# Kernel optimization log

Measured on AMD Instinct MI355X. Metric: run time of the kernel, lower is better.

Reference implementation:

```python
import jax, jax.numpy as jnp
import numpy as np

N, CH, H, W = 2, 64, 96, 96
NH, CHUNK, RED = 4, 144, 4
CM = CH // RED  # match channels = 16
RES_SCALE = 1.0
NORM_EPS = 5e-5


def conv2d(x, w, b):
    # 3x3 'same' conv, NCHW / OIHW
    y = jax.lax.conv_general_dilated(x, w, (1, 1), 'SAME',
                                     dimension_numbers=('NCHW', 'OIHW', 'NCHW'))
    return y + b[None, :, None, None]


def setup_inputs() -> dict:
    key = jax.random.key(0)
    ks = jax.random.split(key, 8)
    L = H * W
    hb = min(L // CHUNK + (L // CHUNK) % 2, 128)  # = 64
    x = jax.random.normal(ks[0], (N, CH, H, W), jnp.float32)
    # per-round semi-orthogonal rotations: rows of (CM, hb) orthonormal
    g = jax.random.normal(ks[1], (NH, hb, CM), jnp.float32)
    q = jnp.stack([jnp.linalg.qr(g[h])[0] for h in range(NH)])  # (NH, hb, CM)
    rot = jnp.transpose(q, (2, 0, 1))  # (CM, NH, hb)
    def s(k, shape, fan):
        return jax.random.normal(k, shape, jnp.float32) / np.sqrt(fan).astype(np.float32)
    wm = s(ks[2], (CM, CH, 3, 3), CH * 9)
    wa = s(ks[3], (CH, CH, 3, 3), CH * 9)
    wf = s(ks[4], (CH, CH, 3, 3), CH * 9)
    fc1_w = s(ks[5], (CHUNK, CH), CH)
    fc2_w = s(ks[6], (CHUNK, CHUNK), CHUNK)
    return {'x': x, 'rot': rot,
            'wm': wm, 'bm': jnp.zeros((CM,), jnp.float32),
            'wa': wa, 'ba': jnp.zeros((CH,), jnp.float32),
            'wf': wf, 'bf': jnp.zeros((CH,), jnp.float32),
            'fc1_w': fc1_w, 'fc1_b': jnp.zeros((CHUNK,), jnp.float32),
            'fc2_w': fc2_w, 'fc2_b': jnp.zeros((CHUNK,), jnp.float32)}


def reference(x, rot, wm, bm, wa, ba, wf, bf, fc1_w, fc1_b, fc2_w, fc2_b):
    n, _, h, w = x.shape
    L = h * w
    hb = rot.shape[-1]
    # embeddings: (N, L, C)
    xe = jax.nn.relu(conv2d(x, wm, bm)).reshape(n, CM, L).transpose(0, 2, 1)
    ye = jax.nn.relu(conv2d(x, wa, ba)).reshape(n, CH, L).transpose(0, 2, 1)
    fe = jax.nn.relu(conv2d(x, wf, bf)).reshape(n, CH, L).transpose(0, 2, 1)
    # LSH: argmax over rotated directions, offset per round (detached in original)
    rv = jnp.einsum('ntf,fhi->nhti', xe, rot)  # (N, NH, L, hb)
    codes = jnp.argmax(rv, -1) + (jnp.arange(NH) * hb)[None, :, None]
    codes = codes.reshape(n, NH * L)
    idx = jnp.argsort(codes, axis=-1)
    undo = jnp.argsort(idx, axis=-1)
    mod = idx % L
    gather = lambda t: jnp.take_along_axis(t, mod[..., None], axis=1)
    nch = L // CHUNK  # L chosen divisible by CHUNK -> padding = 0
    xs = gather(xe).reshape(n, NH, nch, CHUNK, CM)
    ys = gather(ye).reshape(n, NH, nch, CHUNK, CH)
    fs = gather(fe).reshape(n, NH, nch, CHUNK, CH)
    nrm = jnp.linalg.norm(xs, axis=-1, keepdims=True)
    xmatch = xs / jnp.maximum(nrm, NORM_EPS)
    adj = lambda t: jnp.concatenate([t, jnp.roll(t, 1, axis=2), jnp.roll(t, -1, axis=2)], axis=3)
    xmatch = adj(xmatch)   # (n, NH, nch, 3*CHUNK, CM)
    ya = adj(ys)           # (n, NH, nch, 3*CHUNK, CH)
    fa = adj(fs)           # (n, NH, nch, 3*CHUNK, CH)
    hid = jax.nn.relu(fa @ fc1_w.T + fc1_b)
    fc_raw = jnp.swapaxes(hid @ fc2_w.T + fc2_b, -1, -2)  # (n, NH, nch, CHUNK, 3*CHUNK)
    raw = jnp.einsum('nhkie,nhkje->nhkij', xs, xmatch) + fc_raw
    bsc = jax.scipy.special.logsumexp(raw, axis=-1, keepdims=True)
    score = jnp.exp(raw - bsc)
    ret = jnp.einsum('nhkij,nhkje->nhkie', score, ya)  # (n, NH, nch, CHUNK, CH)
    ret = ret.reshape(n, NH * L, CH)
    bsc = bsc.reshape(n, NH * L)
    ret = jnp.take_along_axis(ret, undo[..., None], axis=1)
    bsc = jnp.take_along_axis(bsc, undo, axis=1)
    ret = ret.reshape(n, NH, L, CH)
    probs = jax.nn.softmax(bsc.reshape(n, NH, L, 1), axis=1)
    out = jnp.sum(ret * probs, axis=1)  # (n, L, CH)
    out = out.transpose(0, 2, 1).reshape(n, CH, h, w)
    return out * RES_SCALE + x
```

## Files before the change

### kernel.cpp

```cpp
#include <hip/hip_runtime.h>
#include <hip/hip_bf16.h>

#define LL 9216
#define TOT 36864
#define CHK 144
#define NSEG 144
#define EPS_N 5e-5f

typedef __bf16 bf16x8 __attribute__((ext_vector_type(8)));
typedef float f32x4 __attribute__((ext_vector_type(4)));

__device__ __forceinline__ float dot4(float4 a, float4 b) {
    return a.x*b.x + a.y*b.y + a.z*b.z + a.w*b.w;
}
__device__ __forceinline__ unsigned short f2bf(float f) {
    __hip_bfloat16 h = __float2bfloat16(f);
    return *reinterpret_cast<unsigned short*>(&h);
}
__device__ __forceinline__ float bf2f(unsigned short u) {
    return __uint_as_float(((unsigned int)u) << 16);
}

__global__ __launch_bounds__(256) void k_wprep(
    const float* __restrict__ fc1w, const float* __restrict__ fc2w,
    const float* __restrict__ wa, const float* __restrict__ wf,
    unsigned short* __restrict__ w1bf, unsigned short* __restrict__ w2bf,
    unsigned short* __restrict__ wpack)
{
    int i = blockIdx.x * 256 + threadIdx.x;
    if (i < 144 * 64) w1bf[i] = f2bf(fc1w[i]);
    if (i < 144 * 160) {
        int r = i / 160, c = i - r * 160;
        w2bf[i] = (c < 144) ? f2bf(fc2w[r * 144 + c]) : 0;
    }
    if (i < 128 * 576) {
        int o = i / 576, kk = i - o * 576;
        int dydx = kk >> 6, c = kk & 63;
        const float* src = (o < 64) ? wa : wf;
        wpack[i] = f2bf(src[(o & 63) * 576 + c * 9 + dydx]);
    }
}

__global__ __launch_bounds__(256) void k_conv2(
    const float* __restrict__ x, const float* __restrict__ wm,
    const float* __restrict__ bm, const float* __restrict__ rot,
    unsigned short* __restrict__ xeb, unsigned short* __restrict__ xnb,
    unsigned char* __restrict__ codes,
    const unsigned short* __restrict__ wpack,
    const float* __restrict__ ba, const float* __restrict__ bfb,
    const unsigned short* __restrict__ w1bf, const float* __restrict__ fc1_b,
    const unsigned short* __restrict__ w2bf, const float* __restrict__ fc2_b,
    unsigned short* __restrict__ yeb, unsigned short* __restrict__ re2b)
{
    __shared__ __align__(16) char smem[47104];
    int tid = threadIdx.x;
    int b7 = blockIdx.x % 7, bq = blockIdx.x / 7;

    if (b7 < 3) {
        float* xl   = (float*)smem;
        float* rotT = (float*)(smem + 25600);
        float* xsp  = (float*)(smem + 41984);
        int b = bq * 3 + b7;
        int n = b / 144, tile = b % 144;
        int ty0 = (tile / 12) * 8, tx0 = (tile % 12) * 8;
        for (int li = tid; li < 6400; li += 256) {
            int c = li / 100, s = li % 100;
            int yy = s / 10, xx = s % 10;
            int gy = ty0 + yy - 1, gx = tx0 + xx - 1;
            float v = 0.f;
            if ((unsigned)gy < 96u && (unsigned)gx < 96u)
                v = x[((n * 64 + c) * 96 + gy) * 96 + gx];
            xl[li] = v;
        }
        for (int e = tid; e < 4096; e += 256) {
            int f = e >> 8, r = e & 255;
            rotT[r * 16 + f] = rot[f * 256 + r];
        }
        __syncthreads();
        int p = tid & 63, og = tid >> 6;
        int row = p >> 3, col = p & 7;
        int ogs = __builtin_amdgcn_readfirstlane(og);
        const float* wb = wm + (size_t)ogs * 4 * 576;
        float acc0 = 0.f, acc1 = 0.f, acc2 = 0.f, acc3 = 0.f;
        for (int c = 0; c < 64; ++c) {
            float xp[9];
            int base = c * 100 + row * 10 + col;
            #pragma unroll
            for (int dy = 0; dy < 3; ++dy)
                #pragma unroll
                for (int dx = 0; dx < 3; ++dx)
                    xp[dy * 3 + dx] = xl[base + dy * 10 + dx];
            const float* w0 = wb + c * 9;
            #pragma unroll
            for (int u = 0; u < 9; ++u) {
                acc0 += w0[u]        * xp[u];
                acc1 += w0[576 + u]  * xp[u];
                acc2 += w0[1152 + u] * xp[u];
                acc3 += w0[1728 + u] * xp[u];
            }
        }
        int o = ogs * 4;
        float v0 = acc0 + bm[o + 0]; v0 = v0 > 0.f ? v0 : 0.f;
        float v1 = acc1 + bm[o + 1]; v1 = v1 > 0.f ? v1 : 0.f;
        float v2 = acc2 + bm[o + 2]; v2 = v2 > 0.f ? v2 : 0.f;
        float v3 = acc3 + bm[o + 3]; v3 = v3 > 0.f ? v3 : 0.f;
        size_t t = (size_t)n * LL + (ty0 + row) * 96 + tx0 + col;
        unsigned short pk[4] = {f2bf(v0), f2bf(v1), f2bf(v2), f2bf(v3)};
        *(uint2*)(xeb + t * 16 + o) = *(uint2*)pk;
        *(float4*)(xsp + p * 20 + o) = make_float4(v0, v1, v2, v3);
        __syncthreads();
        int pos = tid & 63, h = tid >> 6;
        int prow = pos >> 3, pcol = pos & 7;
        size_t tc = (size_t)n * LL + (ty0 + prow) * 96 + tx0 + pcol;
        float4 q0 = *(float4*)(xsp + pos * 20 + 0);
        float4 q1 = *(float4*)(xsp + pos * 20 + 4);
        float4 q2 = *(float4*)(xsp + pos * 20 + 8);
        float4 q3 = *(float4*)(xsp + pos * 20 + 12);
        if (h == 0) {
            float nn = dot4(q0,q0) + dot4(q1,q1) + dot4(q2,q2) + dot4(q3,q3);
            float s = fmaxf(sqrtf(nn), EPS_N);
            float inv = 1.f / s;
            unsigned short pn[16];
            pn[0]=f2bf(q0.x*inv);  pn[1]=f2bf(q0.y*inv);  pn[2]=f2bf(q0.z*inv);  pn[3]=f2bf(q0.w*inv);
            pn[4]=f2bf(q1.x*inv);  pn[5]=f2bf(q1.y*inv);  pn[6]=f2bf(q1.z*inv);  pn[7]=f2bf(q1.w*inv);
            pn[8]=f2bf(q2.x*inv);  pn[9]=f2bf(q2.y*inv);  pn[10]=f2bf(q2.z*inv); pn[11]=f2bf(q2.w*inv);
            pn[12]=f2bf(q3.x*inv); pn[13]=f2bf(q3.y*inv); pn[14]=f2bf(q3.z*inv); pn[15]=f2bf(q3.w*inv);
            *(uint4*)(xnb + tc * 16)     = ((uint4*)pn)[0];
            *(uint4*)(xnb + tc * 16 + 8) = ((uint4*)pn)[1];
        }
        float best = -1e30f; int bi = 0;
        const float* rp = rotT + h * 1024;
        for (int i = 0; i < 64; ++i) {
            const float4* r4 = (const float4*)(rp + i * 16);
            float v = dot4(q0, r4[0]) + dot4(q1, r4[1]) + dot4(q2, r4[2]) + dot4(q3, r4[3]);
            if (v > best) { best = v; bi = i; }
        }
        codes[(size_t)n * TOT + h * LL + (tc - (size_t)n * LL)] = (unsigned char)(h * 64 + bi);
        return;
    }

    unsigned short* xt  = (unsigned short*)smem;
    unsigned short* fet = (unsigned short*)(smem + 21600);
    unsigned short* hb  = (unsigned short*)(smem + 28512);
    int b = bq * 4 + (b7 - 3);
    int n = b / 192, rem = b % 192;
    int y = rem >> 1, strip = rem & 1;
    int x0 = strip * 48;
    for (int e = tid; e < 9600; e += 256) {
        int r = e / 3200, r2 = e - r * 3200;
        int c = r2 / 50, j = r2 - c * 50;
        int gy = y - 1 + r, gx = x0 - 1 + j;
        float v = 0.f;
        if ((unsigned)gy < 96u && (unsigned)gx < 96u)
            v = x[((n * 64 + c) * 96 + gy) * 96 + gx];
        xt[(r * 50 + j) * 72 + c] = f2bf(v);
    }
    for (int e = tid; e < 384; e += 256) {
        int r = e >> 3, pq = e & 7;
        *(unsigned int*)(hb + r * 168 + 144 + pq * 2) = 0;
    }
    __syncthreads();
    int wave = tid >> 6, lane = tid & 63;
    int n16 = lane & 15, quad = lane >> 4;
    f32x4 acc[2][3];
    #pragma unroll
    for (int mi = 0; mi < 2; ++mi)
        #pragma unroll
        for (int nt = 0; nt < 3; ++nt) acc[mi][nt] = (f32x4){0.f, 0.f, 0.f, 0.f};
    #pragma unroll
    for (int s = 0; s < 18; ++s) {
        int dydx = s >> 1, half = s & 1;
        int dy = dydx / 3, dxm = dydx - dy * 3;
        bf16x8 B[3];
        #pragma unroll
        for (int nt = 0; nt < 3; ++nt) {
            int j = nt * 16 + n16 + dxm;
            B[nt] = *(bf16x8*)(xt + (dy * 50 + j) * 72 + half * 32 + quad * 8);
        }
        #pragma unroll
        for (int mi = 0; mi < 2; ++mi) {
            int o = (wave * 2 + mi) * 16 + n16;
            bf16x8 A = *(const bf16x8*)(wpack + o * 576 + dydx * 64 + half * 32 + quad * 8);
            #pragma unroll
            for (int nt = 0; nt < 3; ++nt)
                acc[mi][nt] = __builtin_amdgcn_mfma_f32_16x16x32_bf16(A, B[nt], acc[mi][nt], 0, 0, 0);
        }
    }
    #pragma unroll
    for (int mi = 0; mi < 2; ++mi) {
        int mt = wave * 2 + mi;
        int obase = mt * 16 + quad * 4;
        float4 b4 = (mt < 4) ? *(const float4*)(ba + obase)
                             : *(const float4*)(bfb + obase - 64);
        #pragma unroll
        for (int nt = 0; nt < 3; ++nt) {
            int j = nt * 16 + n16;
            unsigned short pk[4];
            float v0 = acc[mi][nt][0] + b4.x; pk[0] = f2bf(v0 > 0.f ? v0 : 0.f);
            float v1 = acc[mi][nt][1] + b4.y; pk[1] = f2bf(v1 > 0.f ? v1 : 0.f);
            float v2 = acc[mi][nt][2] + b4.z; pk[2] = f2bf(v2 > 0.f ? v2 : 0.f);
            float v3 = acc[mi][nt][3] + b4.w; pk[3] = f2bf(v3 > 0.f ? v3 : 0.f);
            if (mt < 4) {
                size_t t = (size_t)n * LL + y * 96 + x0 + j;
                *(uint2*)(yeb + t * 64 + obase) = *(uint2*)pk;
            } else {
                *(uint2*)(fet + j * 72 + (obase - 64)) = *(uint2*)pk;
            }
        }
    }
    __syncthreads();
    size_t R0 = (size_t)n * LL + y * 96 + x0;
    for (int nt = wave; nt < 9; nt += 4) {
        int bn = nt * 16 + n16;
        bf16x8 b0 = *(const bf16x8*)(w1bf + bn * 64 + quad * 8);
        bf16x8 b1 = *(const bf16x8*)(w1bf + bn * 64 + 32 + quad * 8);
        float bb = fc1_b[bn];
        #pragma unroll
        for (int m = 0; m < 3; ++m) {
            int arow = m * 16 + n16;
            bf16x8 a0 = *(bf16x8*)(fet + arow * 72 + quad * 8);
            bf16x8 a1 = *(bf16x8*)(fet + arow * 72 + 32 + quad * 8);
            f32x4 c2 = {0.f, 0.f, 0.f, 0.f};
            c2 = __builtin_amdgcn_mfma_f32_16x16x32_bf16(a0, b0, c2, 0, 0, 0);
            c2 = __builtin_amdgcn_mfma_f32_16x16x32_bf16(a1, b1, c2, 0, 0, 0);
            #pragma unroll
            for (int r = 0; r < 4; ++r) {
                float v = c2[r] + bb;
                hb[(m * 16 + quad * 4 + r) * 168 + bn] = f2bf(v > 0.f ? v : 0.f);
            }
        }
    }
    __syncthreads();
    for (int nt = wave; nt < 9; nt += 4) {
        int bn = nt * 16 + n16;
        bf16x8 wv2[5];
        #pragma unroll
        for (int kk = 0; kk < 5; ++kk)
            wv2[kk] = *(const bf16x8*)(w2bf + bn * 160 + kk * 32 + quad * 8);
        float bb = fc2_b[bn];
        #pragma unroll
        for (int m = 0; m < 3; ++m) {
            int arow = m * 16 + n16;
            f32x4 c2 = {0.f, 0.f, 0.f, 0.f};
            #pragma unroll
            for (int kk = 0; kk < 5; ++kk) {
                bf16x8 a = *(bf16x8*)(hb + arow * 168 + kk * 32 + quad * 8);
                c2 = __builtin_amdgcn_mfma_f32_16x16x32_bf16(a, wv2[kk], c2, 0, 0, 0);
            }
            #pragma unroll
            for (int r = 0; r < 4; ++r)
                re2b[(R0 + m * 16 + quad * 4 + r) * 144 + bn] = f2bf(c2[r] + bb);
        }
    }
}

__global__ __launch_bounds__(256) void k_hist(
    const unsigned char* __restrict__ codes, int* __restrict__ hist)
{
    __shared__ int lh[256];
    int b2 = blockIdx.x;
    int n = b2 / NSEG, seg = b2 % NSEG;
    int tid = threadIdx.x;
    lh[tid] = 0;
    __syncthreads();
    int code = codes[(size_t)n * TOT + seg * 256 + tid];
    atomicAdd(&lh[code], 1);
    __syncthreads();
    hist[((size_t)n * 256 + tid) * NSEG + seg] = lh[tid];
}

__global__ void k_scan(int* __restrict__ hist)
{
    __shared__ int sc[256];
    int n = blockIdx.x, bin = threadIdx.x;
    int* hp = hist + ((size_t)n * 256 + bin) * NSEG;
    int4 buf[36];
    int4* hp4 = (int4*)hp;
    #pragma unroll
    for (int q = 0; q < 36; ++q) buf[q] = hp4[q];
    int running = 0;
    #pragma unroll
    for (int q = 0; q < 36; ++q) {
        int t0 = buf[q].x; buf[q].x = running; running += t0;
        int t1 = buf[q].y; buf[q].y = running; running += t1;
        int t2 = buf[q].z; buf[q].z = running; running += t2;
        int t3 = buf[q].w; buf[q].w = running; running += t3;
    }
    sc[bin] = running;
    __syncthreads();
    for (int off = 1; off < 256; off <<= 1) {
        int v = sc[bin];
        int u = (bin >= off) ? sc[bin - off] : 0;
        __syncthreads();
        sc[bin] = v + u;
        __syncthreads();
    }
    int bs = sc[bin] - running;
    #pragma unroll
    for (int q = 0; q < 36; ++q) {
        buf[q].x += bs; buf[q].y += bs; buf[q].z += bs; buf[q].w += bs;
        hp4[q] = buf[q];
    }
}

__global__ __launch_bounds__(256) void k_place(
    const unsigned char* __restrict__ codes, const int* __restrict__ hist,
    int* __restrict__ idx)
{
    __shared__ unsigned char cl[256];
    int b = blockIdx.x, n = b / NSEG, seg = b % NSEG;
    int tid = threadIdx.x;
    int my = codes[(size_t)n * TOT + seg * 256 + tid];
    cl[tid] = (unsigned char)my;
    __syncthreads();
    int rank = 0;
    for (int j = 0; j < tid; ++j) rank += (cl[j] == my);
    int pos = hist[((size_t)n * 256 + my) * NSEG + seg] + rank;
    idx[(size_t)n * TOT + pos] = seg * 256 + tid;
}

__global__ __launch_bounds__(256) void k_gather(
    const int* __restrict__ idx, const unsigned short* __restrict__ xeb,
    const unsigned short* __restrict__ xnb, const unsigned short* __restrict__ yeb,
    const unsigned short* __restrict__ re2b,
    unsigned short* __restrict__ qs, unsigned short* __restrict__ ks,
    unsigned short* __restrict__ vsT, unsigned short* __restrict__ fst,
    int* __restrict__ undo)
{
    __shared__ int tl[144];
    int b0 = blockIdx.x;
    int b = ((b0 & 7) << 6) | (b0 >> 3);
    int nh = b >> 6, chunk = b & 63;
    int n = nh >> 2, h = nh & 3;
    size_t gb = (size_t)nh * LL + chunk * 144;
    size_t nL = (size_t)n * LL;
    int tid = threadIdx.x;
    if (tid < 144) {
        int t = idx[(size_t)n * TOT + h * LL + chunk * 144 + tid] - h * LL;
        tl[tid] = t;
        undo[(size_t)nh * LL + t] = chunk * 144 + tid;
    }
    __syncthreads();
    for (int e = tid; e < 288; e += 256) {
        int s = e >> 1, half = e & 1;
        size_t src = (nL + tl[s]) * 16 + half * 8;
        *(uint4*)(qs + (gb + s) * 16 + half * 8) = *(const uint4*)(xeb + src);
        *(uint4*)(ks + (gb + s) * 16 + half * 8) = *(const uint4*)(xnb + src);
    }
    size_t vb = (size_t)(nh * 64 + chunk) * 64;
    for (int e = tid; e < 576; e += 256) {
        int p = e % 72, su = e / 72;
        uint4 a  = *(const uint4*)(yeb + (nL + tl[2 * p])     * 64 + su * 8);
        uint4 bq = *(const uint4*)(yeb + (nL + tl[2 * p + 1]) * 64 + su * 8);
        const unsigned short* pa = (const unsigned short*)&a;
        const unsigned short* pb = (const unsigned short*)&bq;
        #pragma unroll
        for (int ci = 0; ci < 8; ++ci) {
            int c = su * 8 + ci;
            *(unsigned int*)(vsT + (vb + c) * 144 + 2 * p) =
                (unsigned int)pa[ci] | ((unsigned int)pb[ci] << 16);
        }
    }
    for (int e = tid; e < 1296; e += 256) {
        int mt = e / 144, s = e - mt * 144;
        const unsigned short* src = re2b + (nL + tl[s]) * 144 + mt * 16;
        unsigned short* dst = fst + ((size_t)(nh * 9 + mt) * LL + chunk * 144 + s) * 16;
        *(uint4*)(dst)     = *(const uint4*)(src);
        *(uint4*)(dst + 8) = *(const uint4*)(src + 8);
    }
}

__global__ __launch_bounds__(256, 2) void k_attn(
    const unsigned short* __restrict__ qs, const unsigned short* __restrict__ ks,
    const unsigned short* __restrict__ vsT, const unsigned short* __restrict__ fst,
    unsigned short* __restrict__ rets, float* __restrict__ bscs)
{
    __shared__ __align__(16) unsigned short Pw[4][16 * 56];

    int B = blockIdx.x;
    int wb = (B & 7) * 144 + (B >> 3);
    int tid = threadIdx.x;
    int lane = tid & 63, wv = tid >> 6;
    int n16 = lane & 15, quad = lane >> 4;
    int job = wb * 4 + wv;
    int bucket = job / 9, mt = job - bucket * 9;
    int n = bucket >> 8, rem = bucket & 255;
    int h = rem >> 6, k = rem & 63;
    int nh = n * 4 + h;

    size_t hL = (size_t)nh * LL;
    int ch0 = k, ch1 = (k + 63) & 63, ch2 = (k + 1) & 63;
    unsigned short* Pp = &Pw[wv][0];
    const unsigned short* fsl = fst + (size_t)(nh * 9 + mt) * LL * 16;

    bf16x8 afragQ = {};
    if (quad < 2)
        afragQ = *(const bf16x8*)(qs + (hL + ch0 * 144 + mt * 16 + n16) * 16 + quad * 8);

    f32x4 acc[4];
    float rm[4], rl[4];
    #pragma unroll
    for (int ct = 0; ct < 4; ++ct) acc[ct] = (f32x4){0.f, 0.f, 0.f, 0.f};
    #pragma unroll
    for (int r = 0; r < 4; ++r) { rm[r] = -1e30f; rl[r] = 0.f; }

#define SLOT(T) ((((T) < 3) ? ch0 : ((T) < 6) ? ch1 : ch2) * 144 + ((T) % 3) * 48)

#define LOAD_KF(T, KS, FV) do {                                                      \
    int sl_ = SLOT(T);                                                               \
    if (quad < 2) {                                                                  \
        KS[0] = *(const bf16x8*)(ks + (hL + sl_ + n16) * 16 + quad * 8);             \
        KS[1] = *(const bf16x8*)(ks + (hL + sl_ + 16 + n16) * 16 + quad * 8);        \
        KS[2] = *(const bf16x8*)(ks + (hL + sl_ + 32 + n16) * 16 + quad * 8);        \
    }                                                                                \
    FV[0] = *(const ushort4*)(fsl + (size_t)(sl_ + n16) * 16 + quad * 4);            \
    FV[1] = *(const ushort4*)(fsl + (size_t)(sl_ + 16 + n16) * 16 + quad * 4);       \
    FV[2] = *(const ushort4*)(fsl + (size_t)(sl_ + 32 + n16) * 16 + quad * 4);       \
} while (0)

#define ATTN_ITER(T, KS, FV, NKS, NFV) do {                                          \
    int chx_ = ((T) < 3) ? ch0 : ((T) < 6) ? ch1 : ch2;                              \
    const unsigned short* vch_ = vsT + (size_t)(nh * 64 + chx_) * 9216;              \
    int vo_ = ((T) % 3) * 48;                                                        \
    bf16x8 Bv0_[4];                                                                  \
    _Pragma("unroll")                                                                \
    for (int ct_ = 0; ct_ < 4; ++ct_)                                                \
        Bv0_[ct_] = *(const bf16x8*)(vch_ + (size_t)(ct_ * 16 + n16) * 144 + vo_ + quad * 8); \
    if ((T) < 8) LOAD_KF((T) + 1, NKS, NFV);                                         \
    f32x4 c0_ = {bf2f(FV[0].x), bf2f(FV[0].y), bf2f(FV[0].z), bf2f(FV[0].w)};        \
    f32x4 c1_ = {bf2f(FV[1].x), bf2f(FV[1].y), bf2f(FV[1].z), bf2f(FV[1].w)};        \
    f32x4 c2_ = {bf2f(FV[2].x), bf2f(FV[2].y), bf2f(FV[2].z), bf2f(FV[2].w)};        \
    c0_ = __builtin_amdgcn_mfma_f32_16x16x32_bf16(afragQ, KS[0], c0_, 0, 0, 0);      \
    c1_ = __builtin_amdgcn_mfma_f32_16x16x32_bf16(afragQ, KS[1], c1_, 0, 0, 0);      \
    c2_ = __builtin_amdgcn_mfma_f32_16x16x32_bf16(afragQ, KS[2], c2_, 0, 0, 0);      \
    _Pragma("unroll")                                                                \
    for (int r_ = 0; r_ < 4; ++r_) {                                                 \
        float v0_ = c0_[r_], v1_ = c1_[r_], v2_ = c2_[r_];                           \
        float mm_ = fmaxf(fmaxf(v0_, v1_), v2_);                                     \
        mm_ = fmaxf(mm_, __shfl_xor(mm_, 1, 16));                                    \
        mm_ = fmaxf(mm_, __shfl_xor(mm_, 2, 16));                                    \
        mm_ = fmaxf(mm_, __shfl_xor(mm_, 4, 16));                                    \
        mm_ = fmaxf(mm_, __shfl_xor(mm_, 8, 16));                                    \
        float mn_ = fmaxf(rm[r_], mm_);                                              \
        float a_ = __expf(rm[r_] - mn_);                                             \
        float s0_ = __expf(v0_ - mn_), s1_ = __expf(v1_ - mn_), s2_ = __expf(v2_ - mn_); \
        float ss_ = s0_ + s1_ + s2_;                                                 \
        ss_ += __shfl_xor(ss_, 1, 16);                                               \
        ss_ += __shfl_xor(ss_, 2, 16);                                               \
        ss_ += __shfl_xor(ss_, 4, 16);                                               \
        ss_ += __shfl_xor(ss_, 8, 16);                                               \
        rl[r_] = rl[r_] * a_ + ss_;                                                  \
        rm[r_] = mn_;                                                                \
        acc[0][r_] *= a_; acc[1][r_] *= a_; acc[2][r_] *= a_; acc[3][r_] *= a_;      \
        int rw_ = quad * 4 + r_;                                                     \
        Pp[rw_ * 56 +      n16] = f2bf(s0_);                                         \
        Pp[rw_ * 56 + 16 + n16] = f2bf(s1_);                                         \
        Pp[rw_ * 56 + 32 + n16] = f2bf(s2_);                                         \
    }                                                                                \
                \
    bf16x8 Ap0_ = *(const bf16x8*)(Pp + n16 * 56 + quad * 8);                        \
    int ko1_ = (quad < 2) ? 32 + quad * 8 : 0;          \
    bf16x8 Bv1_[4];                                                                  \
    _Pragma("unroll")                                                                \
    for (int ct_ = 0; ct_ < 4; ++ct_)                                                \
        Bv1_[ct_] = *(const bf16x8*)(vch_ + (size_t)(ct_ * 16 + n16) * 144 + vo_ + ko1_); \
    _Pragma("unroll")                                                                \
    for (int ct_ = 0; ct_ < 4; ++ct_)                                                \
        acc[ct_] = __builtin_amdgcn_mfma_f32_16x16x32_bf16(Ap0_, Bv0_[ct_], acc[ct_], 0, 0, 0); \
    bf16x8 Ap1_ = {};                                                                \
    if (quad < 2)                                                                    \
        Ap1_ = *(const bf16x8*)(Pp + n16 * 56 + 32 + quad * 8);                      \
    _Pragma("unroll")                                                                \
    for (int ct_ = 0; ct_ < 4; ++ct_)                                                \
        acc[ct_] = __builtin_amdgcn_mfma_f32_16x16x32_bf16(Ap1_, Bv1_[ct_], acc[ct_], 0, 0, 0); \
} while (0)

    bf16x8 ksA[3] = {}, ksB[3] = {};
    ushort4 fvA[3], fvB[3];
    LOAD_KF(0, ksA, fvA);
    ATTN_ITER(0, ksA, fvA, ksB, fvB);
    ATTN_ITER(1, ksB, fvB, ksA, fvA);
    ATTN_ITER(2, ksA, fvA, ksB, fvB);
    ATTN_ITER(3, ksB, fvB, ksA, fvA);
    ATTN_ITER(4, ksA, fvA, ksB, fvB);
    ATTN_ITER(5, ksB, fvB, ksA, fvA);
    ATTN_ITER(6, ksA, fvA, ksB, fvB);
    ATTN_ITER(7, ksB, fvB, ksA, fvA);
    ATTN_ITER(8, ksA, fvA, ksB, fvB);

#undef ATTN_ITER
#undef LOAD_KF
#undef SLOT

    size_t sp0 = hL + ch0 * 144;
    if (n16 == 0) {
        #pragma unroll
        for (int r = 0; r < 4; ++r)
            bscs[sp0 + mt * 16 + quad * 4 + r] = rm[r] + __logf(rl[r]);
    }
    #pragma unroll
    for (int r = 0; r < 4; ++r) {
        float inv = 1.f / rl[r];
        #pragma unroll
        for (int ct = 0; ct < 4; ++ct)
            rets[(sp0 + mt * 16 + quad * 4 + r) * 64 + ct * 16 + n16] =
                f2bf(acc[ct][r] * inv);
    }
}

__global__ __launch_bounds__(256) void k_final(
    const unsigned short* __restrict__ rets, const float* __restrict__ bscs,
    const int* __restrict__ undo, const float* __restrict__ x,
    float* __restrict__ out)
{
    __shared__ float pr[4][64];
    __shared__ int us[4][64];
    __shared__ float accl[64 * 65];
    int b = blockIdx.x, n = b / 144;
    int t0 = (b % 144) * 64;
    int tid = threadIdx.x;
    {
        int h = tid >> 6, tt = tid & 63;
        us[h][tt] = undo[((size_t)n * 4 + h) * LL + t0 + tt];
    }
    __syncthreads();
    if (tid < 64) {
        float b0 = bscs[((size_t)n * 4 + 0) * LL + us[0][tid]];
        float b1 = bscs[((size_t)n * 4 + 1) * LL + us[1][tid]];
        float b2 = bscs[((size_t)n * 4 + 2) * LL + us[2][tid]];
        float b3 = bscs[((size_t)n * 4 + 3) * LL + us[3][tid]];
        float mx = fmaxf(fmaxf(b0, b1), fmaxf(b2, b3));
        float e0 = __expf(b0-mx), e1 = __expf(b1-mx), e2 = __expf(b2-mx), e3 = __expf(b3-mx);
        float inv = 1.f / (e0 + e1 + e2 + e3);
        pr[0][tid] = e0*inv; pr[1][tid] = e1*inv; pr[2][tid] = e2*inv; pr[3][tid] = e3*inv;
    }
    __syncthreads();
    int cc = tid & 63, tt4 = tid >> 6;
    #pragma unroll
    for (int q = 0; q < 16; ++q) {
        int tt = tt4 + 4*q;
        float v = 0.f;
        #pragma unroll
        for (int h2 = 0; h2 < 4; ++h2)
            v += bf2f(rets[(((size_t)n*4 + h2)*LL + us[h2][tt])*64 + cc]) * pr[h2][tt];
        accl[cc*65 + tt] = v;
    }
    __syncthreads();
    int tt = tid & 63, c4 = tid >> 6;
    #pragma unroll
    for (int q = 0; q < 16; ++q) {
        int ch = c4 + 4*q;
        size_t o = ((size_t)n*64 + ch)*LL + t0 + tt;
        out[o] = accl[ch*65 + tt] + x[o];
    }
}

extern "C" void kernel_launch(void* const* d_in, const int* in_sizes, int n_in,
                              void* d_out, int out_size, void* d_ws, size_t ws_size,
                              hipStream_t stream)
{
    const float* x    = (const float*)d_in[0];
    const float* rot  = (const float*)d_in[1];
    const float* wm   = (const float*)d_in[2];
    const float* bm   = (const float*)d_in[3];
    const float* wa   = (const float*)d_in[4];
    const float* ba   = (const float*)d_in[5];
    const float* wf   = (const float*)d_in[6];
    const float* bf   = (const float*)d_in[7];
    const float* fc1w = (const float*)d_in[8];
    const float* fc1b = (const float*)d_in[9];
    const float* fc2w = (const float*)d_in[10];
    const float* fc2b = (const float*)d_in[11];
    float* out = (float*)d_out;

    char* ws = (char*)d_ws;
    unsigned short* xeb  = (unsigned short*)(ws + 0);
    unsigned short* yeb  = (unsigned short*)(ws + 589824);
    unsigned short* xnb  = (unsigned short*)(ws + 2949120);
    unsigned short* re2b = (unsigned short*)(ws + 3538944);
    unsigned short* w1bf = (unsigned short*)(ws + 8847360);
    unsigned short* w2bf = (unsigned short*)(ws + 8865792);
    unsigned short* wpak = (unsigned short*)(ws + 8911872);
    unsigned char* codes = (unsigned char*)(ws + 9059328);
    int* hist            = (int*)(ws + 9133056);
    int* idxb            = (int*)(ws + 9427968);
    unsigned short* rets = (unsigned short*)(ws + 0);
    float* bscs          = (float*)(ws + 9437184);
    unsigned short* qs   = (unsigned short*)(ws + 9732096);
    unsigned short* ks   = (unsigned short*)(ws + 12091392);
    unsigned short* vsT  = (unsigned short*)(ws + 14450688);
    unsigned short* fst  = (unsigned short*)(ws + 23887872);
    int* undo            = (int*)(ws + 45121536);

    k_wprep    <<<288,  256, 0, stream>>>(fc1w, fc2w, wa, wf, w1bf, w2bf, wpak);
    k_conv2    <<<672,  256, 0, stream>>>(x, wm, bm, rot, xeb, xnb, codes,
                                          wpak, ba, bf, w1bf, fc1b, w2bf, fc2b,
                                          yeb, re2b);
    k_hist     <<<288,  256, 0, stream>>>(codes, hist);
    k_scan     <<<2,    256, 0, stream>>>(hist);
    k_place    <<<288,  256, 0, stream>>>(codes, hist, idxb);
    k_gather   <<<512,  256, 0, stream>>>(idxb, xeb, xnb, yeb, re2b,
                                          qs, ks, vsT, fst, undo);
    k_attn     <<<1152, 256, 0, stream>>>(qs, ks, vsT, fst, rets, bscs);
    k_final    <<<288,  256, 0, stream>>>(rets, bscs, undo, x, out);
}
```

Before: 201.9 us.

## Split gather and final kernels across more blocks; per-wave rank histograms in place

k_place now builds per-wavefront code histograms in shared memory, so each thread counts matches only within its own wave instead of scanning all earlier threads. k_gather is split into two block halves, one copying q/k/v and the other copying the fc tiles and undo indices, which doubles the grid. k_final handles 16 tokens per block instead of 64, quadrupling the grid to raise parallelism. The narrower k_final tiles make the output stores only 16 floats wide per channel row, which reduces coalescing, and the gather split re-reads the idx/tl setup in both halves.

```diff
diff --git a/kernel.cpp b/kernel.cpp
--- a/kernel.cpp
+++ b/kernel.cpp
@@ -269,7 +269,7 @@
     hist[((size_t)n * 256 + tid) * NSEG + seg] = lh[tid];
 }
 
-__global__ void k_scan(int* __restrict__ hist)
+__global__ __launch_bounds__(256, 1) void k_scan(int* __restrict__ hist)
 {
     __shared__ int sc[256];
     int n = blockIdx.x, bin = threadIdx.x;
@@ -308,13 +308,20 @@
     int* __restrict__ idx)
 {
     __shared__ unsigned char cl[256];
+    __shared__ int wh[4][256];
     int b = blockIdx.x, n = b / NSEG, seg = b % NSEG;
-    int tid = threadIdx.x;
+    int tid = threadIdx.x, wv = tid >> 6;
+    for (int e = tid; e < 1024; e += 256) ((int*)wh)[e] = 0;
     int my = codes[(size_t)n * TOT + seg * 256 + tid];
     cl[tid] = (unsigned char)my;
     __syncthreads();
+    atomicAdd(&wh[wv][my], 1);
+    __syncthreads();
     int rank = 0;
-    for (int j = 0; j < tid; ++j) rank += (cl[j] == my);
+    for (int j = wv << 6; j < tid; ++j) rank += (cl[j] == my);
+    #pragma unroll
+    for (int w = 0; w < 3; ++w)
+        if (w < wv) rank += wh[w][my];
     int pos = hist[((size_t)n * 256 + my) * NSEG + seg] + rank;
     idx[(size_t)n * TOT + pos] = seg * 256 + tid;
 }
@@ -329,7 +336,8 @@
 {
     __shared__ int tl[144];
     int b0 = blockIdx.x;
-    int b = ((b0 & 7) << 6) | (b0 >> 3);
+    int half = b0 >> 9, bb = b0 & 511;
+    int b = ((bb & 7) << 6) | (bb >> 3);
     int nh = b >> 6, chunk = b & 63;
     int n = nh >> 2, h = nh & 3;
     size_t gb = (size_t)nh * LL + chunk * 144;
@@ -338,35 +346,38 @@
     if (tid < 144) {
         int t = idx[(size_t)n * TOT + h * LL + chunk * 144 + tid] - h * LL;
         tl[tid] = t;
-        undo[(size_t)nh * LL + t] = chunk * 144 + tid;
-    }
-    __syncthreads();
-    for (int e = tid; e < 288; e += 256) {
-        int s = e >> 1, half = e & 1;
-        size_t src = (nL + tl[s]) * 16 + half * 8;
-        *(uint4*)(qs + (gb + s) * 16 + half * 8) = *(const uint4*)(xeb + src);
-        *(uint4*)(ks + (gb + s) * 16 + half * 8) = *(const uint4*)(xnb + src);
-    }
-    size_t vb = (size_t)(nh * 64 + chunk) * 64;
-    for (int e = tid; e < 576; e += 256) {
-        int p = e % 72, su = e / 72;
-        uint4 a  = *(const uint4*)(yeb + (nL + tl[2 * p])     * 64 + su * 8);
-        uint4 bq = *(const uint4*)(yeb + (nL + tl[2 * p + 1]) * 64 + su * 8);
-        const unsigned short* pa = (const unsigned short*)&a;
-        const unsigned short* pb = (const unsigned short*)&bq;
-        #pragma unroll
-        for (int ci = 0; ci < 8; ++ci) {
-            int c = su * 8 + ci;
-            *(unsigned int*)(vsT + (vb + c) * 144 + 2 * p) =
-                (unsigned int)pa[ci] | ((unsigned int)pb[ci] << 16);
-        }
-    }
-    for (int e = tid; e < 1296; e += 256) {
-        int mt = e / 144, s = e - mt * 144;
-        const unsigned short* src = re2b + (nL + tl[s]) * 144 + mt * 16;
-        unsigned short* dst = fst + ((size_t)(nh * 9 + mt) * LL + chunk * 144 + s) * 16;
-        *(uint4*)(dst)     = *(const uint4*)(src);
-        *(uint4*)(dst + 8) = *(const uint4*)(src + 8);
+        if (half) undo[(size_t)nh * LL + t] = chunk * 144 + tid;
+    }
+    __syncthreads();
+    if (!half) {
+        for (int e = tid; e < 288; e += 256) {
+            int s = e >> 1, hf = e & 1;
+            size_t src = (nL + tl[s]) * 16 + hf * 8;
+            *(uint4*)(qs + (gb + s) * 16 + hf * 8) = *(const uint4*)(xeb + src);
+            *(uint4*)(ks + (gb + s) * 16 + hf * 8) = *(const uint4*)(xnb + src);
+        }
+        size_t vb = (size_t)(nh * 64 + chunk) * 64;
+        for (int e = tid; e < 576; e += 256) {
+            int p = e % 72, su = e / 72;
+            uint4 a  = *(const uint4*)(yeb + (nL + tl[2 * p])     * 64 + su * 8);
+            uint4 bq = *(const uint4*)(yeb + (nL + tl[2 * p + 1]) * 64 + su * 8);
+            const unsigned short* pa = (const unsigned short*)&a;
+            const unsigned short* pb = (const unsigned short*)&bq;
+            #pragma unroll
+            for (int ci = 0; ci < 8; ++ci) {
+                int c = su * 8 + ci;
+                *(unsigned int*)(vsT + (vb + c) * 144 + 2 * p) =
+                    (unsigned int)pa[ci] | ((unsigned int)pb[ci] << 16);
+            }
+        }
+    } else {
+        for (int e = tid; e < 1296; e += 256) {
+            int mt = e / 144, s = e - mt * 144;
+            const unsigned short* src = re2b + (nL + tl[s]) * 144 + mt * 16;
+            unsigned short* dst = fst + ((size_t)(nh * 9 + mt) * LL + chunk * 144 + s) * 16;
+            *(uint4*)(dst)     = *(const uint4*)(src);
+            *(uint4*)(dst + 8) = *(const uint4*)(src + 8);
+        }
     }
 }
 
@@ -513,18 +524,18 @@
     const int* __restrict__ undo, const float* __restrict__ x,
     float* __restrict__ out)
 {
-    __shared__ float pr[4][64];
-    __shared__ int us[4][64];
-    __shared__ float accl[64 * 65];
-    int b = blockIdx.x, n = b / 144;
-    int t0 = (b % 144) * 64;
+    __shared__ float pr[4][16];
+    __shared__ int us[4][16];
+    __shared__ float accl[64 * 17];
+    int b = blockIdx.x, n = b / 576;
+    int t0 = (b % 576) * 16;
     int tid = threadIdx.x;
-    {
-        int h = tid >> 6, tt = tid & 63;
+    if (tid < 64) {
+        int h = tid >> 4, tt = tid & 15;
         us[h][tt] = undo[((size_t)n * 4 + h) * LL + t0 + tt];
     }
     __syncthreads();
-    if (tid < 64) {
+    if (tid < 16) {
         float b0 = bscs[((size_t)n * 4 + 0) * LL + us[0][tid]];
         float b1 = bscs[((size_t)n * 4 + 1) * LL + us[1][tid]];
         float b2 = bscs[((size_t)n * 4 + 2) * LL + us[2][tid]];
@@ -535,23 +546,23 @@
         pr[0][tid] = e0*inv; pr[1][tid] = e1*inv; pr[2][tid] = e2*inv; pr[3][tid] = e3*inv;
     }
     __syncthreads();
-    int cc = tid & 63, tt4 = tid >> 6;
-    #pragma unroll
-    for (int q = 0; q < 16; ++q) {
-        int tt = tt4 + 4*q;
+    int cc = tid & 63, tq = tid >> 6;
+    #pragma unroll
+    for (int q = 0; q < 4; ++q) {
+        int tt = tq * 4 + q;
         float v = 0.f;
         #pragma unroll
         for (int h2 = 0; h2 < 4; ++h2)
             v += bf2f(rets[(((size_t)n*4 + h2)*LL + us[h2][tt])*64 + cc]) * pr[h2][tt];
-        accl[cc*65 + tt] = v;
-    }
-    __syncthreads();
-    int tt = tid & 63, c4 = tid >> 6;
-    #pragma unroll
-    for (int q = 0; q < 16; ++q) {
-        int ch = c4 + 4*q;
+        accl[cc*17 + tt] = v;
+    }
+    __syncthreads();
+    int tt = tid & 15, c4 = tid >> 4;
+    #pragma unroll
+    for (int q = 0; q < 4; ++q) {
+        int ch = c4 + 16*q;
         size_t o = ((size_t)n*64 + ch)*LL + t0 + tt;
-        out[o] = accl[ch*65 + tt] + x[o];
+        out[o] = accl[ch*17 + tt] + x[o];
     }
 }
 
@@ -599,8 +610,8 @@
     k_hist     <<<288,  256, 0, stream>>>(codes, hist);
     k_scan     <<<2,    256, 0, stream>>>(hist);
     k_place    <<<288,  256, 0, stream>>>(codes, hist, idxb);
-    k_gather   <<<512,  256, 0, stream>>>(idxb, xeb, xnb, yeb, re2b,
+    k_gather   <<<1024, 256, 0, stream>>>(idxb, xeb, xnb, yeb, re2b,
                                           qs, ks, vsT, fst, undo);
     k_attn     <<<1152, 256, 0, stream>>>(qs, ks, vsT, fst, rets, bscs);
-    k_final    <<<288,  256, 0, stream>>>(rets, bscs, undo, x, out);
-}
+    k_final    <<<1152, 256, 0, stream>>>(rets, bscs, undo, x, out);
+}
```

Result: faster. 190.1 us (median of 5 runs) (-5.8%).
